# Kernel tuning notes

Hardware: AMD Instinct MI355X
Metric: run time of the kernel (lower is better)

The kernel has to match this reference:

```python
import jax, jax.numpy as jnp
import numpy as np

EMBED_DIM = 1024
NUM_HEADS = 16
RANK = 32
HEAD_DIM = EMBED_DIM // NUM_HEADS
SCALE = 1.0 / np.sqrt(RANK).astype(np.float32)


def setup_inputs() -> dict:
    key = jax.random.key(0)
    ks = jax.random.split(key, 9)
    B, S = 2, 2048
    def lin(k, fan_in, fan_out):
        bound = 1.0 / np.sqrt(fan_in)
        return jax.random.uniform(k, (fan_in, fan_out), jnp.float32, -bound, bound)
    return {
        "hidden_states": jax.random.normal(ks[0], (B, S, EMBED_DIM), jnp.float32),
        "Wq": lin(ks[1], EMBED_DIM, RANK * NUM_HEADS),
        "bq": jnp.zeros((RANK * NUM_HEADS,), jnp.float32),
        "Wk": lin(ks[2], EMBED_DIM, RANK * NUM_HEADS),
        "bk": jnp.zeros((RANK * NUM_HEADS,), jnp.float32),
        "Wv": lin(ks[3], EMBED_DIM, EMBED_DIM),
        "bv": jnp.zeros((EMBED_DIM,), jnp.float32),
        "Wo": lin(ks[4], EMBED_DIM, EMBED_DIM),
        "bo": jnp.zeros((EMBED_DIM,), jnp.float32),
    }


def reference(hidden_states, Wq, bq, Wk, bk, Wv, bv, Wo, bo):
    B, S, E = hidden_states.shape
    q = (hidden_states @ Wq + bq).reshape(B, S, NUM_HEADS, RANK)      # [b,i,h,r]
    k = (hidden_states @ Wk + bk).reshape(B, S, NUM_HEADS, RANK)      # [b,j,h,r]
    v = (hidden_states @ Wv + bv).reshape(B, S, NUM_HEADS, HEAD_DIM)  # [b,j,h,d]
    # full [b,i,j,h] score tensor, softmax over j (axis=2), as in the torch code
    scores = jnp.einsum('bihr,bjhr->bijh', q, k) * SCALE
    attn = jax.nn.softmax(scores, axis=2)
    out = jnp.einsum('bijh,bjhd->bihd', attn, v).reshape(B, S, E)
    return out @ Wo + bo
```

## Files before the change

### kernel.cpp

```cpp
#include <hip/hip_runtime.h>

#define EMBED   1024
#define NHEADS  16
#define RANK    32
#define HDIM    64
#define BATCH   2
#define SEQ     2048
#define BSQ     (BATCH * SEQ)
#define CEXP    0.25505998f

typedef __attribute__((ext_vector_type(8))) short bf16x8;
typedef __attribute__((ext_vector_type(4))) float f32x4;

__device__ __forceinline__ float bf2f(unsigned short u) {
    union { unsigned int i; float f; } x; x.i = ((unsigned int)u) << 16;
    return x.f;
}
__device__ __forceinline__ unsigned short f2bf(float f) {
    union { float f; unsigned int i; } x; x.f = f;
    unsigned int r = x.i + 0x7FFFu + ((x.i >> 16) & 1u);
    return (unsigned short)(r >> 16);
}

#define ASYNC16(gp, lp) \
    __builtin_amdgcn_global_load_lds( \
        (const __attribute__((address_space(1))) void*)(gp), \
        (__attribute__((address_space(3))) void*)(lp), 16, 0, 0)

__global__ __launch_bounds__(256) void prep_all(
    const float* __restrict__ hs,
    const float* __restrict__ Wq, const float* __restrict__ Wk,
    const float* __restrict__ Wv, const float* __restrict__ Wo,
    const float* __restrict__ bq, const float* __restrict__ bk,
    const float* __restrict__ bv,
    unsigned short* __restrict__ hsb, unsigned short* __restrict__ wT_all,
    unsigned short* __restrict__ woT, float* __restrict__ ball)
{
    __shared__ float L[64][65];
    const int blk = blockIdx.x;
    const int t = threadIdx.x;

    if (blk < 2048) {
        const size_t i = ((size_t)blk * 256 + t) * 8;
        float4 v0 = *(const float4*)(hs + i);
        float4 v1 = *(const float4*)(hs + i + 4);
        ushort4 o0, o1;
        o0.x = f2bf(v0.x); o0.y = f2bf(v0.y); o0.z = f2bf(v0.z); o0.w = f2bf(v0.w);
        o1.x = f2bf(v1.x); o1.y = f2bf(v1.y); o1.z = f2bf(v1.z); o1.w = f2bf(v1.w);
        *(ushort4*)(hsb + i) = o0;
        *(ushort4*)(hsb + i + 4) = o1;
        return;
    }
    if (blk < 2816) {
        int idx = blk - 2048;
        int z, bx, by;
        if (idx < 256) { z = idx >> 7; int r2 = idx & 127; bx = r2 & 7; by = r2 >> 3; }
        else { idx -= 256; z = 2 + (idx >> 8); int r2 = idx & 255; bx = r2 & 15; by = r2 >> 4; }
        const int Nw = (z < 2) ? 512 : 1024;
        const float* W = (z == 0) ? Wq : (z == 1) ? Wk : (z == 2) ? Wv : Wo;
        unsigned short* dst = (z == 3) ? woT : (wT_all + (size_t)z * 512 * 1024);

        const int r = t >> 2, c0 = (t & 3) * 16;
        const float* src = W + (size_t)(by * 64 + r) * Nw + bx * 64 + c0;
        #pragma unroll
        for (int u = 0; u < 4; u++)
            *(float4*)&L[r][c0 + 4 * u] = *(const float4*)(src + 4 * u);
        __syncthreads();
        unsigned short* drow = dst + (size_t)(bx * 64 + r) * 1024 + by * 64 + c0;
        #pragma unroll
        for (int u4 = 0; u4 < 4; u4++) {
            ushort4 o;
            o.x = f2bf(L[c0 + 4 * u4 + 0][r]);
            o.y = f2bf(L[c0 + 4 * u4 + 1][r]);
            o.z = f2bf(L[c0 + 4 * u4 + 2][r]);
            o.w = f2bf(L[c0 + 4 * u4 + 3][r]);
            *(ushort4*)(drow + 4 * u4) = o;
        }
        return;
    }
    {
        const int i = (blk - 2816) * 256 + t;
        ball[i] = (i < 512) ? bq[i] : (i < 1024) ? bk[i - 512] : bv[i - 1024];
    }
}

__global__ __launch_bounds__(256) void gemm_qkv(
    const unsigned short* __restrict__ A, const unsigned short* __restrict__ BT,
    const float* __restrict__ bias,
    unsigned short* __restrict__ qH, unsigned short* __restrict__ kH,
    unsigned short* __restrict__ vTout)
{
    __shared__ unsigned short As[128 * 32];
    __shared__ unsigned short Bs[128 * 32];
    const int K = 1024;
    const int t = threadIdx.x;
    const int lane = t & 63;
    const int li = lane & 15, la = lane >> 4;
    const int w = t >> 6, wm = w >> 1, wn = w & 1;
    const int row0 = blockIdx.y * 128, col0 = blockIdx.x * 128;

    const int sr = lane >> 2, sc2 = (lane & 3) * 8;
    const unsigned short* ag0 = A + (size_t)(row0 + w * 32 + sr) * K + sc2;
    const unsigned short* ag1 = A + (size_t)(row0 + w * 32 + 16 + sr) * K + sc2;
    const unsigned short* bg0 = BT + (size_t)(col0 + w * 32 + sr) * K + sc2;
    const unsigned short* bg1 = BT + (size_t)(col0 + w * 32 + 16 + sr) * K + sc2;
    unsigned short* lA0 = &As[(w * 32) * 32];
    unsigned short* lA1 = &As[(w * 32 + 16) * 32];
    unsigned short* lB0 = &Bs[(w * 32) * 32];
    unsigned short* lB1 = &Bs[(w * 32 + 16) * 32];

    f32x4 acc[4][4];
    #pragma unroll
    for (int i = 0; i < 4; i++)
        #pragma unroll
        for (int j = 0; j < 4; j++)
            acc[i][j] = (f32x4){0.f, 0.f, 0.f, 0.f};

    for (int k0 = 0; k0 < K; k0 += 32) {
        ASYNC16(ag0 + k0, lA0);
        ASYNC16(ag1 + k0, lA1);
        ASYNC16(bg0 + k0, lB0);
        ASYNC16(bg1 + k0, lB1);
        __syncthreads();
        bf16x8 af[4], bfr[4];
        #pragma unroll
        for (int mt = 0; mt < 4; mt++)
            af[mt] = *(const bf16x8*)&As[(wm * 64 + mt * 16 + li) * 32 + la * 8];
        #pragma unroll
        for (int nt = 0; nt < 4; nt++)
            bfr[nt] = *(const bf16x8*)&Bs[(wn * 64 + nt * 16 + li) * 32 + la * 8];
        #pragma unroll
        for (int mt = 0; mt < 4; mt++)
            #pragma unroll
            for (int nt = 0; nt < 4; nt++)
                acc[mt][nt] = __builtin_amdgcn_mfma_f32_16x16x32_bf16(af[mt], bfr[nt], acc[mt][nt], 0, 0, 0);
        __syncthreads();
    }

    const int bb = row0 >> 11;
    const int jb = (row0 & 2047) + wm * 64;
    #pragma unroll
    for (int nt = 0; nt < 4; nt++) {
        const int col = col0 + wn * 64 + nt * 16 + li;
        const float bval = bias[col];
        if (col < 1024) {
            const int hh = (col & 511) >> 5;
            const int rr = col & 31;
            unsigned short* base = ((col < 512) ? qH : kH)
                + ((size_t)(bb * 16 + hh) * 2048) * 32 + rr;
            #pragma unroll
            for (int mt = 0; mt < 4; mt++)
                #pragma unroll
                for (int r = 0; r < 4; r++)
                    base[(size_t)(jb + mt * 16 + la * 4 + r) * 32] =
                        f2bf(acc[mt][nt][r] + bval);
        } else {
            const int hd = col - 1024;
            unsigned short* dcol = vTout + ((size_t)(bb * 16 + (hd >> 6)) * 64 + (hd & 63)) * SEQ;
            #pragma unroll
            for (int mt = 0; mt < 4; mt++) {
                const int srow = jb + mt * 16 + la * 4;
                ushort4 o;
                o.x = f2bf(acc[mt][nt][0] + bval);
                o.y = f2bf(acc[mt][nt][1] + bval);
                o.z = f2bf(acc[mt][nt][2] + bval);
                o.w = f2bf(acc[mt][nt][3] + bval);
                *(ushort4*)(dcol + srow) = o;
            }
        }
    }
}

__global__ __launch_bounds__(256) void gemm_out(
    const unsigned short* __restrict__ A, const unsigned short* __restrict__ BT,
    const float* __restrict__ bias, float* __restrict__ C)
{
    __shared__ unsigned short As[64 * 32];
    __shared__ unsigned short Bs[128 * 32];
    const int K = 1024;
    const int t = threadIdx.x;
    const int lane = t & 63;
    const int li = lane & 15, la = lane >> 4;
    const int w = t >> 6, wm = w >> 1, wn = w & 1;
    const int row0 = blockIdx.y * 64, col0 = blockIdx.x * 128;

    const int sr = lane >> 2, sc2 = (lane & 3) * 8;
    const unsigned short* ag0 = A + (size_t)(row0 + w * 16 + sr) * K + sc2;
    const unsigned short* bg0 = BT + (size_t)(col0 + w * 32 + sr) * K + sc2;
    const unsigned short* bg1 = BT + (size_t)(col0 + w * 32 + 16 + sr) * K + sc2;
    unsigned short* lA0 = &As[(w * 16) * 32];
    unsigned short* lB0 = &Bs[(w * 32) * 32];
    unsigned short* lB1 = &Bs[(w * 32 + 16) * 32];

    f32x4 acc[2][4];
    #pragma unroll
    for (int i = 0; i < 2; i++)
        #pragma unroll
        for (int j = 0; j < 4; j++)
            acc[i][j] = (f32x4){0.f, 0.f, 0.f, 0.f};

    for (int k0 = 0; k0 < K; k0 += 32) {
        ASYNC16(ag0 + k0, lA0);
        ASYNC16(bg0 + k0, lB0);
        ASYNC16(bg1 + k0, lB1);
        __syncthreads();
        bf16x8 af[2], bfr[4];
        #pragma unroll
        for (int mt = 0; mt < 2; mt++)
            af[mt] = *(const bf16x8*)&As[(wm * 32 + mt * 16 + li) * 32 + la * 8];
        #pragma unroll
        for (int nt = 0; nt < 4; nt++)
            bfr[nt] = *(const bf16x8*)&Bs[(wn * 64 + nt * 16 + li) * 32 + la * 8];
        #pragma unroll
        for (int mt = 0; mt < 2; mt++)
            #pragma unroll
            for (int nt = 0; nt < 4; nt++)
                acc[mt][nt] = __builtin_amdgcn_mfma_f32_16x16x32_bf16(af[mt], bfr[nt], acc[mt][nt], 0, 0, 0);
        __syncthreads();
    }

    #pragma unroll
    for (int nt = 0; nt < 4; nt++) {
        const int col = col0 + wn * 64 + nt * 16 + li;
        const float bval = bias[col];
        #pragma unroll
        for (int mt = 0; mt < 2; mt++)
            #pragma unroll
            for (int r = 0; r < 4; r++) {
                const int row = row0 + wm * 32 + mt * 16 + la * 4 + r;
                C[(size_t)row * 1024 + col] = acc[mt][nt][r] + bval;
            }
    }
}

__global__ __launch_bounds__(256) void attn_v6(
    const unsigned short* __restrict__ qH,
    const unsigned short* __restrict__ kH,
    const unsigned short* __restrict__ vT,
    unsigned short* __restrict__ ao)
{
    __shared__ unsigned short kt[64 * 48];
    __shared__ unsigned short vt[64 * 72];
    __shared__ unsigned short P[128 * 72];

    const int t = threadIdx.x;
    const int lane = t & 63;
    const int li = lane & 15, la = lane >> 4;
    const int w = t >> 6;

    const int bh = blockIdx.x & 31;
    const int itile = blockIdx.x >> 5;
    const int i0 = itile * 128;
    const int b = bh >> 4, h = bh & 15;

    bf16x8 qf[2];
    #pragma unroll
    for (int it = 0; it < 2; it++) {
        const unsigned short* qp = qH + ((size_t)bh * 2048 + i0 + w * 32 + it * 16 + li) * 32 + la * 8;
        ushort4 q0 = *(const ushort4*)qp;
        ushort4 q1 = *(const ushort4*)(qp + 4);
        short u[8];
        u[0] = (short)f2bf(bf2f(q0.x) * CEXP);
        u[1] = (short)f2bf(bf2f(q0.y) * CEXP);
        u[2] = (short)f2bf(bf2f(q0.z) * CEXP);
        u[3] = (short)f2bf(bf2f(q0.w) * CEXP);
        u[4] = (short)f2bf(bf2f(q1.x) * CEXP);
        u[5] = (short)f2bf(bf2f(q1.y) * CEXP);
        u[6] = (short)f2bf(bf2f(q1.z) * CEXP);
        u[7] = (short)f2bf(bf2f(q1.w) * CEXP);
        qf[it] = *(const bf16x8*)u;
    }

    bf16x8 vones;
    #pragma unroll
    for (int u2 = 0; u2 < 8; u2++) vones[u2] = (short)0x3F80;

    const unsigned short* kbase = kH + (size_t)bh * 2048 * 32;
    const unsigned short* vbase = vT + (size_t)bh * 64 * SEQ;

    const int kr = t >> 2, kc = (t & 3) * 8;
    const int vr = t >> 3, vc = (t & 7) * 8;

    f32x4 accO[2][4], accl[2];
    #pragma unroll
    for (int mt = 0; mt < 2; mt++) {
        accl[mt] = (f32x4){0.f, 0.f, 0.f, 0.f};
        #pragma unroll
        for (int dt = 0; dt < 4; dt++) accO[mt][dt] = (f32x4){0.f, 0.f, 0.f, 0.f};
    }

    uint4 kreg  = *(const uint4*)(kbase + (size_t)kr * 32 + kc);
    uint4 vreg0 = *(const uint4*)(vbase + (size_t)vr * SEQ + vc);
    uint4 vreg1 = *(const uint4*)(vbase + (size_t)(vr + 32) * SEQ + vc);

    for (int j0 = 0; j0 < SEQ; j0 += 64) {
        __syncthreads();
        *(uint4*)&kt[kr * 48 + kc] = kreg;
        *(uint4*)&vt[vr * 72 + vc] = vreg0;
        *(uint4*)&vt[(vr + 32) * 72 + vc] = vreg1;
        __syncthreads();

        const int jn = (j0 + 64) & 2047;
        kreg  = *(const uint4*)(kbase + (size_t)(jn + kr) * 32 + kc);
        vreg0 = *(const uint4*)(vbase + (size_t)vr * SEQ + jn + vc);
        vreg1 = *(const uint4*)(vbase + (size_t)(vr + 32) * SEQ + jn + vc);

        f32x4 sc[4][2];
        #pragma unroll
        for (int jt = 0; jt < 4; jt++) {
            const bf16x8 kf = *(const bf16x8*)&kt[(jt * 16 + li) * 48 + la * 8];
            sc[jt][0] = __builtin_amdgcn_mfma_f32_16x16x32_bf16(kf, qf[0], (f32x4){0.f,0.f,0.f,0.f}, 0, 0, 0);
            sc[jt][1] = __builtin_amdgcn_mfma_f32_16x16x32_bf16(kf, qf[1], (f32x4){0.f,0.f,0.f,0.f}, 0, 0, 0);
        }

        #pragma unroll
        for (int jt = 0; jt < 4; jt++)
            #pragma unroll
            for (int it = 0; it < 2; it++) {
                union { float f; unsigned int u; } c0, c1, c2, c3;
                c0.f = exp2f(sc[jt][it][0]);
                c1.f = exp2f(sc[jt][it][1]);
                c2.f = exp2f(sc[jt][it][2]);
                c3.f = exp2f(sc[jt][it][3]);
                uint2 pk;
                pk.x = __builtin_amdgcn_perm(c1.u + 0x8000u, c0.u + 0x8000u, 0x07060302u);
                pk.y = __builtin_amdgcn_perm(c3.u + 0x8000u, c2.u + 0x8000u, 0x07060302u);
                *(uint2*)&P[(w * 32 + it * 16 + li) * 72 + jt * 16 + la * 4] = pk;
            }

        #pragma unroll
        for (int mt = 0; mt < 2; mt++) {
            #pragma unroll
            for (int ks = 0; ks < 2; ks++) {
                const bf16x8 pf = *(const bf16x8*)&P[(w * 32 + mt * 16 + li) * 72 + ks * 32 + la * 8];
                accl[mt] = __builtin_amdgcn_mfma_f32_16x16x32_bf16(pf, vones, accl[mt], 0, 0, 0);
                #pragma unroll
                for (int dt = 0; dt < 4; dt++) {
                    const bf16x8 vf = *(const bf16x8*)&vt[(dt * 16 + li) * 72 + ks * 32 + la * 8];
                    accO[mt][dt] = __builtin_amdgcn_mfma_f32_16x16x32_bf16(pf, vf, accO[mt][dt], 0, 0, 0);
                }
            }
        }
    }

    #pragma unroll
    for (int mt = 0; mt < 2; mt++) {
        float linv[4];
        #pragma unroll
        for (int r = 0; r < 4; r++) linv[r] = 1.f / accl[mt][r];
        #pragma unroll
        for (int dt = 0; dt < 4; dt++)
            #pragma unroll
            for (int r = 0; r < 4; r++) {
                const int row = b * SEQ + i0 + w * 32 + mt * 16 + la * 4 + r;
                ao[(size_t)row * 1024 + h * 64 + dt * 16 + li] = f2bf(accO[mt][dt][r] * linv[r]);
            }
    }
}

extern "C" void kernel_launch(void* const* d_in, const int* in_sizes, int n_in,
                              void* d_out, int out_size, void* d_ws, size_t ws_size,
                              hipStream_t stream) {
    const float* hs = (const float*)d_in[0];
    const float* Wq = (const float*)d_in[1];
    const float* bq = (const float*)d_in[2];
    const float* Wk = (const float*)d_in[3];
    const float* bk = (const float*)d_in[4];
    const float* Wv = (const float*)d_in[5];
    const float* bv = (const float*)d_in[6];
    const float* Wo = (const float*)d_in[7];
    const float* bo = (const float*)d_in[8];

    char* p = (char*)d_ws;
    unsigned short* hsb = (unsigned short*)(p);
    unsigned short* wT  = (unsigned short*)(p + 8388608u);
    unsigned short* woT = (unsigned short*)(p + 12582912u);
    float*          ball= (float*)(p + 14680064u);
    unsigned short* qHb = (unsigned short*)(p + 14688256u);
    unsigned short* kHb = (unsigned short*)(p + 18882560u);
    unsigned short* vTb = (unsigned short*)(p + 23076864u);
    unsigned short* ao  = (unsigned short*)(p + 31465472u);

    prep_all<<<dim3(2824), 256, 0, stream>>>(hs, Wq, Wk, Wv, Wo, bq, bk, bv,
                                             hsb, wT, woT, ball);

    gemm_qkv<<<dim3(16, 32), 256, 0, stream>>>(hsb, wT, ball, qHb, kHb, vTb);

    attn_v6<<<dim3(512), 256, 0, stream>>>(qHb, kHb, vTb, ao);

    gemm_out<<<dim3(8, 64), 256, 0, stream>>>(ao, woT, bo, (float*)d_out);
}
```

Baseline: 198.6 us.

## Double-buffer attention K/V tiles and shrink GEMM tiles for more blocks

The attention kernel now keeps two shared-memory buffers for K and V, so each step writes the next tile while computing on the current one. This drops one of the two barriers per 64-key step. Both projection GEMMs use narrower 64-column tiles, which doubles the number of workgroups and cuts per-block register use, giving more parallelism on the many CUs. In exchange, the GEMMs get less operand reuse per block and load more from global memory and LDS, and the attention kernel uses more shared memory.

```diff
diff --git a/kernel.cpp b/kernel.cpp
--- a/kernel.cpp
+++ b/kernel.cpp
@@ -91,27 +91,25 @@
     unsigned short* __restrict__ vTout)
 {
     __shared__ unsigned short As[128 * 32];
-    __shared__ unsigned short Bs[128 * 32];
+    __shared__ unsigned short Bs[64 * 32];
     const int K = 1024;
     const int t = threadIdx.x;
     const int lane = t & 63;
     const int li = lane & 15, la = lane >> 4;
-    const int w = t >> 6, wm = w >> 1, wn = w & 1;
-    const int row0 = blockIdx.y * 128, col0 = blockIdx.x * 128;
+    const int w = t >> 6;
+    const int row0 = blockIdx.y * 128, col0 = blockIdx.x * 64;
 
     const int sr = lane >> 2, sc2 = (lane & 3) * 8;
     const unsigned short* ag0 = A + (size_t)(row0 + w * 32 + sr) * K + sc2;
     const unsigned short* ag1 = A + (size_t)(row0 + w * 32 + 16 + sr) * K + sc2;
-    const unsigned short* bg0 = BT + (size_t)(col0 + w * 32 + sr) * K + sc2;
-    const unsigned short* bg1 = BT + (size_t)(col0 + w * 32 + 16 + sr) * K + sc2;
+    const unsigned short* bg0 = BT + (size_t)(col0 + w * 16 + sr) * K + sc2;
     unsigned short* lA0 = &As[(w * 32) * 32];
     unsigned short* lA1 = &As[(w * 32 + 16) * 32];
-    unsigned short* lB0 = &Bs[(w * 32) * 32];
-    unsigned short* lB1 = &Bs[(w * 32 + 16) * 32];
-
-    f32x4 acc[4][4];
-    #pragma unroll
-    for (int i = 0; i < 4; i++)
+    unsigned short* lB0 = &Bs[(w * 16) * 32];
+
+    f32x4 acc[2][4];
+    #pragma unroll
+    for (int i = 0; i < 2; i++)
         #pragma unroll
         for (int j = 0; j < 4; j++)
             acc[i][j] = (f32x4){0.f, 0.f, 0.f, 0.f};
@@ -120,17 +118,16 @@
         ASYNC16(ag0 + k0, lA0);
         ASYNC16(ag1 + k0, lA1);
         ASYNC16(bg0 + k0, lB0);
-        ASYNC16(bg1 + k0, lB1);
-        __syncthreads();
-        bf16x8 af[4], bfr[4];
-        #pragma unroll
-        for (int mt = 0; mt < 4; mt++)
-            af[mt] = *(const bf16x8*)&As[(wm * 64 + mt * 16 + li) * 32 + la * 8];
+        __syncthreads();
+        bf16x8 af[2], bfr[4];
+        #pragma unroll
+        for (int mt = 0; mt < 2; mt++)
+            af[mt] = *(const bf16x8*)&As[(w * 32 + mt * 16 + li) * 32 + la * 8];
         #pragma unroll
         for (int nt = 0; nt < 4; nt++)
-            bfr[nt] = *(const bf16x8*)&Bs[(wn * 64 + nt * 16 + li) * 32 + la * 8];
-        #pragma unroll
-        for (int mt = 0; mt < 4; mt++)
+            bfr[nt] = *(const bf16x8*)&Bs[(nt * 16 + li) * 32 + la * 8];
+        #pragma unroll
+        for (int mt = 0; mt < 2; mt++)
             #pragma unroll
             for (int nt = 0; nt < 4; nt++)
                 acc[mt][nt] = __builtin_amdgcn_mfma_f32_16x16x32_bf16(af[mt], bfr[nt], acc[mt][nt], 0, 0, 0);
@@ -138,10 +135,10 @@
     }
 
     const int bb = row0 >> 11;
-    const int jb = (row0 & 2047) + wm * 64;
+    const int jb = (row0 & 2047) + w * 32;
     #pragma unroll
     for (int nt = 0; nt < 4; nt++) {
-        const int col = col0 + wn * 64 + nt * 16 + li;
+        const int col = col0 + nt * 16 + li;
         const float bval = bias[col];
         if (col < 1024) {
             const int hh = (col & 511) >> 5;
@@ -149,7 +146,7 @@
             unsigned short* base = ((col < 512) ? qH : kH)
                 + ((size_t)(bb * 16 + hh) * 2048) * 32 + rr;
             #pragma unroll
-            for (int mt = 0; mt < 4; mt++)
+            for (int mt = 0; mt < 2; mt++)
                 #pragma unroll
                 for (int r = 0; r < 4; r++)
                     base[(size_t)(jb + mt * 16 + la * 4 + r) * 32] =
@@ -158,7 +155,7 @@
             const int hd = col - 1024;
             unsigned short* dcol = vTout + ((size_t)(bb * 16 + (hd >> 6)) * 64 + (hd & 63)) * SEQ;
             #pragma unroll
-            for (int mt = 0; mt < 4; mt++) {
+            for (int mt = 0; mt < 2; mt++) {
                 const int srow = jb + mt * 16 + la * 4;
                 ushort4 o;
                 o.x = f2bf(acc[mt][nt][0] + bval);
@@ -176,71 +173,59 @@
     const float* __restrict__ bias, float* __restrict__ C)
 {
     __shared__ unsigned short As[64 * 32];
-    __shared__ unsigned short Bs[128 * 32];
+    __shared__ unsigned short Bs[64 * 32];
     const int K = 1024;
     const int t = threadIdx.x;
     const int lane = t & 63;
     const int li = lane & 15, la = lane >> 4;
-    const int w = t >> 6, wm = w >> 1, wn = w & 1;
-    const int row0 = blockIdx.y * 64, col0 = blockIdx.x * 128;
+    const int w = t >> 6;
+    const int row0 = blockIdx.y * 64, col0 = blockIdx.x * 64;
 
     const int sr = lane >> 2, sc2 = (lane & 3) * 8;
     const unsigned short* ag0 = A + (size_t)(row0 + w * 16 + sr) * K + sc2;
-    const unsigned short* bg0 = BT + (size_t)(col0 + w * 32 + sr) * K + sc2;
-    const unsigned short* bg1 = BT + (size_t)(col0 + w * 32 + 16 + sr) * K + sc2;
+    const unsigned short* bg0 = BT + (size_t)(col0 + w * 16 + sr) * K + sc2;
     unsigned short* lA0 = &As[(w * 16) * 32];
-    unsigned short* lB0 = &Bs[(w * 32) * 32];
-    unsigned short* lB1 = &Bs[(w * 32 + 16) * 32];
-
-    f32x4 acc[2][4];
-    #pragma unroll
-    for (int i = 0; i < 2; i++)
-        #pragma unroll
-        for (int j = 0; j < 4; j++)
-            acc[i][j] = (f32x4){0.f, 0.f, 0.f, 0.f};
+    unsigned short* lB0 = &Bs[(w * 16) * 32];
+
+    f32x4 acc[4];
+    #pragma unroll
+    for (int j = 0; j < 4; j++) acc[j] = (f32x4){0.f, 0.f, 0.f, 0.f};
 
     for (int k0 = 0; k0 < K; k0 += 32) {
         ASYNC16(ag0 + k0, lA0);
         ASYNC16(bg0 + k0, lB0);
-        ASYNC16(bg1 + k0, lB1);
-        __syncthreads();
-        bf16x8 af[2], bfr[4];
-        #pragma unroll
-        for (int mt = 0; mt < 2; mt++)
-            af[mt] = *(const bf16x8*)&As[(wm * 32 + mt * 16 + li) * 32 + la * 8];
+        __syncthreads();
+        bf16x8 af, bfr[4];
+        af = *(const bf16x8*)&As[(w * 16 + li) * 32 + la * 8];
         #pragma unroll
         for (int nt = 0; nt < 4; nt++)
-            bfr[nt] = *(const bf16x8*)&Bs[(wn * 64 + nt * 16 + li) * 32 + la * 8];
-        #pragma unroll
-        for (int mt = 0; mt < 2; mt++)
-            #pragma unroll
-            for (int nt = 0; nt < 4; nt++)
-                acc[mt][nt] = __builtin_amdgcn_mfma_f32_16x16x32_bf16(af[mt], bfr[nt], acc[mt][nt], 0, 0, 0);
+            bfr[nt] = *(const bf16x8*)&Bs[(nt * 16 + li) * 32 + la * 8];
+        #pragma unroll
+        for (int nt = 0; nt < 4; nt++)
+            acc[nt] = __builtin_amdgcn_mfma_f32_16x16x32_bf16(af, bfr[nt], acc[nt], 0, 0, 0);
         __syncthreads();
     }
 
     #pragma unroll
     for (int nt = 0; nt < 4; nt++) {
-        const int col = col0 + wn * 64 + nt * 16 + li;
+        const int col = col0 + nt * 16 + li;
         const float bval = bias[col];
         #pragma unroll
-        for (int mt = 0; mt < 2; mt++)
-            #pragma unroll
-            for (int r = 0; r < 4; r++) {
-                const int row = row0 + wm * 32 + mt * 16 + la * 4 + r;
-                C[(size_t)row * 1024 + col] = acc[mt][nt][r] + bval;
-            }
-    }
-}
-
-__global__ __launch_bounds__(256) void attn_v6(
+        for (int r = 0; r < 4; r++) {
+            const int row = row0 + w * 16 + la * 4 + r;
+            C[(size_t)row * 1024 + col] = acc[nt][r] + bval;
+        }
+    }
+}
+
+__global__ __launch_bounds__(256) void attn_v7(
     const unsigned short* __restrict__ qH,
     const unsigned short* __restrict__ kH,
     const unsigned short* __restrict__ vT,
     unsigned short* __restrict__ ao)
 {
-    __shared__ unsigned short kt[64 * 48];
-    __shared__ unsigned short vt[64 * 72];
+    __shared__ unsigned short kt[2][64 * 48];
+    __shared__ unsigned short vt[2][64 * 72];
     __shared__ unsigned short P[128 * 72];
 
     const int t = threadIdx.x;
@@ -275,11 +260,11 @@
     #pragma unroll
     for (int u2 = 0; u2 < 8; u2++) vones[u2] = (short)0x3F80;
 
-    const unsigned short* kbase = kH + (size_t)bh * 2048 * 32;
-    const unsigned short* vbase = vT + (size_t)bh * 64 * SEQ;
-
     const int kr = t >> 2, kc = (t & 3) * 8;
     const int vr = t >> 3, vc = (t & 7) * 8;
+    const unsigned short* kp = kH + (size_t)bh * 2048 * 32 + (size_t)kr * 32 + kc;
+    const unsigned short* vp0 = vT + (size_t)bh * 64 * SEQ + (size_t)vr * SEQ + vc;
+    const unsigned short* vp1 = vp0 + (size_t)32 * SEQ;
 
     f32x4 accO[2][4], accl[2];
     #pragma unroll
@@ -289,59 +274,67 @@
         for (int dt = 0; dt < 4; dt++) accO[mt][dt] = (f32x4){0.f, 0.f, 0.f, 0.f};
     }
 
-    uint4 kreg  = *(const uint4*)(kbase + (size_t)kr * 32 + kc);
-    uint4 vreg0 = *(const uint4*)(vbase + (size_t)vr * SEQ + vc);
-    uint4 vreg1 = *(const uint4*)(vbase + (size_t)(vr + 32) * SEQ + vc);
-
-    for (int j0 = 0; j0 < SEQ; j0 += 64) {
-        __syncthreads();
-        *(uint4*)&kt[kr * 48 + kc] = kreg;
-        *(uint4*)&vt[vr * 72 + vc] = vreg0;
-        *(uint4*)&vt[(vr + 32) * 72 + vc] = vreg1;
-        __syncthreads();
-
-        const int jn = (j0 + 64) & 2047;
-        kreg  = *(const uint4*)(kbase + (size_t)(jn + kr) * 32 + kc);
-        vreg0 = *(const uint4*)(vbase + (size_t)vr * SEQ + jn + vc);
-        vreg1 = *(const uint4*)(vbase + (size_t)(vr + 32) * SEQ + jn + vc);
-
-        f32x4 sc[4][2];
-        #pragma unroll
-        for (int jt = 0; jt < 4; jt++) {
-            const bf16x8 kf = *(const bf16x8*)&kt[(jt * 16 + li) * 48 + la * 8];
-            sc[jt][0] = __builtin_amdgcn_mfma_f32_16x16x32_bf16(kf, qf[0], (f32x4){0.f,0.f,0.f,0.f}, 0, 0, 0);
-            sc[jt][1] = __builtin_amdgcn_mfma_f32_16x16x32_bf16(kf, qf[1], (f32x4){0.f,0.f,0.f,0.f}, 0, 0, 0);
-        }
-
-        #pragma unroll
-        for (int jt = 0; jt < 4; jt++)
-            #pragma unroll
-            for (int it = 0; it < 2; it++) {
-                union { float f; unsigned int u; } c0, c1, c2, c3;
-                c0.f = exp2f(sc[jt][it][0]);
-                c1.f = exp2f(sc[jt][it][1]);
-                c2.f = exp2f(sc[jt][it][2]);
-                c3.f = exp2f(sc[jt][it][3]);
-                uint2 pk;
-                pk.x = __builtin_amdgcn_perm(c1.u + 0x8000u, c0.u + 0x8000u, 0x07060302u);
-                pk.y = __builtin_amdgcn_perm(c3.u + 0x8000u, c2.u + 0x8000u, 0x07060302u);
-                *(uint2*)&P[(w * 32 + it * 16 + li) * 72 + jt * 16 + la * 4] = pk;
-            }
-
-        #pragma unroll
-        for (int mt = 0; mt < 2; mt++) {
-            #pragma unroll
-            for (int ks = 0; ks < 2; ks++) {
-                const bf16x8 pf = *(const bf16x8*)&P[(w * 32 + mt * 16 + li) * 72 + ks * 32 + la * 8];
-                accl[mt] = __builtin_amdgcn_mfma_f32_16x16x32_bf16(pf, vones, accl[mt], 0, 0, 0);
-                #pragma unroll
-                for (int dt = 0; dt < 4; dt++) {
-                    const bf16x8 vf = *(const bf16x8*)&vt[(dt * 16 + li) * 72 + ks * 32 + la * 8];
-                    accO[mt][dt] = __builtin_amdgcn_mfma_f32_16x16x32_bf16(pf, vf, accO[mt][dt], 0, 0, 0);
-                }
-            }
-        }
-    }
+    uint4 kreg  = *(const uint4*)(kp);
+    uint4 vreg0 = *(const uint4*)(vp0);
+    uint4 vreg1 = *(const uint4*)(vp1);
+    *(uint4*)&kt[0][kr * 48 + kc] = kreg;
+    *(uint4*)&vt[0][vr * 72 + vc] = vreg0;
+    *(uint4*)&vt[0][(vr + 32) * 72 + vc] = vreg1;
+    kreg  = *(const uint4*)(kp + 64 * 32);
+    vreg0 = *(const uint4*)(vp0 + 64);
+    vreg1 = *(const uint4*)(vp1 + 64);
+
+    #define ATTN_BODY(BUF, OTHER, JPRE)                                            \
+    {                                                                              \
+        __syncthreads();                                                           \
+        *(uint4*)&kt[OTHER][kr * 48 + kc] = kreg;                                  \
+        *(uint4*)&vt[OTHER][vr * 72 + vc] = vreg0;                                 \
+        *(uint4*)&vt[OTHER][(vr + 32) * 72 + vc] = vreg1;                          \
+        const int jn = (JPRE) & 2047;                                              \
+        kreg  = *(const uint4*)(kp + (size_t)jn * 32);                             \
+        vreg0 = *(const uint4*)(vp0 + jn);                                         \
+        vreg1 = *(const uint4*)(vp1 + jn);                                         \
+        f32x4 sc[4][2];                                                            \
+        _Pragma("unroll")                                                          \
+        for (int jt = 0; jt < 4; jt++) {                                           \
+            const bf16x8 kf = *(const bf16x8*)&kt[BUF][(jt * 16 + li) * 48 + la * 8]; \
+            sc[jt][0] = __builtin_amdgcn_mfma_f32_16x16x32_bf16(kf, qf[0], (f32x4){0.f,0.f,0.f,0.f}, 0, 0, 0); \
+            sc[jt][1] = __builtin_amdgcn_mfma_f32_16x16x32_bf16(kf, qf[1], (f32x4){0.f,0.f,0.f,0.f}, 0, 0, 0); \
+        }                                                                          \
+        _Pragma("unroll")                                                          \
+        for (int jt = 0; jt < 4; jt++)                                             \
+            _Pragma("unroll")                                                      \
+            for (int it = 0; it < 2; it++) {                                       \
+                union { float f; unsigned int u; } c0, c1, c2, c3;                 \
+                c0.f = exp2f(sc[jt][it][0]);                                       \
+                c1.f = exp2f(sc[jt][it][1]);                                       \
+                c2.f = exp2f(sc[jt][it][2]);                                       \
+                c3.f = exp2f(sc[jt][it][3]);                                       \
+                uint2 pk;                                                          \
+                pk.x = __builtin_amdgcn_perm(c1.u + 0x8000u, c0.u + 0x8000u, 0x07060302u); \
+                pk.y = __builtin_amdgcn_perm(c3.u + 0x8000u, c2.u + 0x8000u, 0x07060302u); \
+                *(uint2*)&P[(w * 32 + it * 16 + li) * 72 + jt * 16 + la * 4] = pk; \
+            }                                                                      \
+        _Pragma("unroll")                                                          \
+        for (int mt = 0; mt < 2; mt++) {                                           \
+            _Pragma("unroll")                                                      \
+            for (int ks = 0; ks < 2; ks++) {                                       \
+                const bf16x8 pf = *(const bf16x8*)&P[(w * 32 + mt * 16 + li) * 72 + ks * 32 + la * 8]; \
+                accl[mt] = __builtin_amdgcn_mfma_f32_16x16x32_bf16(pf, vones, accl[mt], 0, 0, 0); \
+                _Pragma("unroll")                                                  \
+                for (int dt = 0; dt < 4; dt++) {                                   \
+                    const bf16x8 vf = *(const bf16x8*)&vt[BUF][(dt * 16 + li) * 72 + ks * 32 + la * 8]; \
+                    accO[mt][dt] = __builtin_amdgcn_mfma_f32_16x16x32_bf16(pf, vf, accO[mt][dt], 0, 0, 0); \
+                }                                                                  \
+            }                                                                      \
+        }                                                                          \
+    }
+
+    for (int j0 = 0; j0 < SEQ; j0 += 128) {
+        ATTN_BODY(0, 1, j0 + 128)
+        ATTN_BODY(1, 0, j0 + 192)
+    }
+    #undef ATTN_BODY
 
     #pragma unroll
     for (int mt = 0; mt < 2; mt++) {
@@ -384,9 +377,9 @@
     prep_all<<<dim3(2824), 256, 0, stream>>>(hs, Wq, Wk, Wv, Wo, bq, bk, bv,
                                              hsb, wT, woT, ball);
 
-    gemm_qkv<<<dim3(16, 32), 256, 0, stream>>>(hsb, wT, ball, qHb, kHb, vTb);
-
-    attn_v6<<<dim3(512), 256, 0, stream>>>(qHb, kHb, vTb, ao);
-
-    gemm_out<<<dim3(8, 64), 256, 0, stream>>>(ao, woT, bo, (float*)d_out);
-}
+    gemm_qkv<<<dim3(32, 32), 256, 0, stream>>>(hsb, wT, ball, qHb, kHb, vTb);
+
+    attn_v7<<<dim3(512), 256, 0, stream>>>(qHb, kHb, vTb, ao);
+
+    gemm_out<<<dim3(16, 64), 256, 0, stream>>>(ao, woT, bo, (float*)d_out);
+}
```

Measured after the change: 196.2 us. Within noise of the previous version (-1.2%).
